# Optimization experiments

Hardware: AMD Instinct MI355X
Metric: run time of the kernel (lower is better)

The kernel has to match this reference:

```python
import jax, jax.numpy as jnp
import numpy as np

D_MODEL = 1024
N_HEADS = 16
D_HEAD = D_MODEL // N_HEADS


def setup_inputs() -> dict:
    key = jax.random.key(0)
    k1, k2, k3, k4, k5 = jax.random.split(key, 5)
    B, S = 2, 2048
    scale_in = 1.0 / np.sqrt(D_MODEL)
    return {
        "x": jax.random.normal(k1, (B, S, D_MODEL), dtype=jnp.float32),
        "qkv_w": jax.random.normal(k2, (3 * D_MODEL, D_MODEL), dtype=jnp.float32) * scale_in,
        "qkv_b": jax.random.normal(k3, (3 * D_MODEL,), dtype=jnp.float32) * 0.02,
        "out_w": jax.random.normal(k4, (D_MODEL, D_MODEL), dtype=jnp.float32) * scale_in,
        "out_b": jax.random.normal(k5, (D_MODEL,), dtype=jnp.float32) * 0.02,
    }


def reference(x, qkv_w, qkv_b, out_w, out_b) -> jnp.ndarray:
    B, S, D = x.shape
    # qkv projection: torch Linear stores weight as (out, in)
    qkv = x @ qkv_w.T + qkv_b                      # [B,S,3D]
    qkv = qkv.reshape(B, S, 3, N_HEADS, D_HEAD)
    qkv = jnp.transpose(qkv, (2, 0, 3, 1, 4))      # [3,B,H,S,d]
    q, k, v = qkv[0], qkv[1], qkv[2]
    scale = 1.0 / np.sqrt(D_HEAD).astype(np.float32)
    scores = jnp.einsum("bhsd,bhtd->bhst", q, k) * scale  # [B,H,S,S]
    attn = jax.nn.softmax(scores, axis=-1)
    out = jnp.einsum("bhst,bhtd->bhsd", attn, v)   # [B,H,S,d]
    out = jnp.transpose(out, (0, 2, 1, 3)).reshape(B, S, D)
    return out @ out_w.T + out_b
```

## Files before the change

### kernel.cpp

```cpp
#include <hip/hip_runtime.h>

typedef __bf16 bf16;
typedef __bf16 bf16x4 __attribute__((ext_vector_type(4)));
typedef __bf16 bf16x8 __attribute__((ext_vector_type(8)));
typedef float  f32x4  __attribute__((ext_vector_type(4)));

__device__ __forceinline__ void gld16(const void* g, void* l) {
  __builtin_amdgcn_global_load_lds(
      (const __attribute__((address_space(1))) void*)g,
      (__attribute__((address_space(3))) void*)l, 16, 0, 0);
}

__global__ void f2bf_all(const float* __restrict__ x, bf16* __restrict__ xo,
                         const float* __restrict__ w1, bf16* __restrict__ w1o,
                         const float* __restrict__ w2, bf16* __restrict__ w2o) {
  int i = blockIdx.x * blockDim.x + threadIdx.x;
  const float* in; bf16* out; int idx;
  if (i < 1048576)      { in = x;  out = xo;  idx = i; }
  else if (i < 1835008) { in = w1; out = w1o; idx = i - 1048576; }
  else                  { in = w2; out = w2o; idx = i - 1835008; }
  float4 v = reinterpret_cast<const float4*>(in)[idx];
  bf16x4 o = { (bf16)v.x, (bf16)v.y, (bf16)v.z, (bf16)v.w };
  reinterpret_cast<bf16x4*>(out)[idx] = o;
}

template<int MODE, int BN>
__global__ __launch_bounds__(256)
void gemm_bt(const bf16* __restrict__ A, const bf16* __restrict__ B,
             const float* __restrict__ bias, void* __restrict__ Cout,
             int K, int N) {
  __shared__ bf16 As[128 * 64];
  __shared__ bf16 Bs[BN * 64];
  const int tid  = threadIdx.x;
  const int wave = tid >> 6, lane = tid & 63;
  const int quad = lane >> 4, l16 = lane & 15;
  const int bm = blockIdx.x * 128, bn = blockIdx.y * BN;
  constexpr int NI  = (BN == 128) ? 4 : 2;
  constexpr int BCH = BN / 32;
  const int wr = (BN == 128) ? (wave >> 1) * 64 : wave * 32;
  const int wc = (BN == 128) ? (wave & 1) * 64 : 0;
  const int arow = lane >> 3;
  const int acol = (lane & 7) * 8;

  f32x4 acc[NI][4] = {};

  const bf16* Ab = A + (size_t)bm * K;
  const bf16* Bb = B + (size_t)bn * K;

  for (int k0 = 0; k0 < K; k0 += 64) {
#pragma unroll
    for (int i = 0; i < 4; ++i) {
      int c = wave * 4 + i;
      gld16(Ab + (size_t)(c * 8 + arow) * K + k0 + acol, As + c * 512);
    }
#pragma unroll
    for (int i = 0; i < BCH; ++i) {
      int c = wave * BCH + i;
      gld16(Bb + (size_t)(c * 8 + arow) * K + k0 + acol, Bs + c * 512);
    }
    __syncthreads();
#pragma unroll
    for (int kk = 0; kk < 64; kk += 32) {
      bf16x8 af[NI], bfr[4];
#pragma unroll
      for (int i = 0; i < NI; ++i)
        af[i]  = *(const bf16x8*)(As + (wr + i * 16 + l16) * 64 + kk + quad * 8);
#pragma unroll
      for (int j = 0; j < 4; ++j)
        bfr[j] = *(const bf16x8*)(Bs + (wc + j * 16 + l16) * 64 + kk + quad * 8);
#pragma unroll
      for (int i = 0; i < NI; ++i)
#pragma unroll
        for (int j = 0; j < 4; ++j)
          acc[i][j] = __builtin_amdgcn_mfma_f32_16x16x32_bf16(af[i], bfr[j], acc[i][j], 0, 0, 0);
    }
    __syncthreads();
  }

  if constexpr (MODE == 0) {
    bf16* Q = (bf16*)Cout;
#pragma unroll
    for (int j = 0; j < 4; ++j) {
      int col = bn + wc + j * 16 + l16;
      float bv  = bias[col];
      int sec = col >> 10, rem = col & 1023;
      int h = rem >> 6, d = rem & 63;
      if (sec < 2) {
        float scl = (sec == 0) ? 0.125f * 1.44269504f : 1.0f;
#pragma unroll
        for (int i = 0; i < NI; ++i) {
#pragma unroll
          for (int r = 0; r < 4; ++r) {
            int row = bm + wr + i * 16 + quad * 4 + r;
            int b = row >> 11, si = row & 2047;
            float v = (acc[i][j][r] + bv) * scl;
            Q[(((size_t)sec * 32 + b * 16 + h) * 2048 + si) * 64 + d] = (bf16)v;
          }
        }
      } else {
#pragma unroll
        for (int i = 0; i < NI; ++i) {
          int row0 = bm + wr + i * 16 + quad * 4;
          int b = row0 >> 11, si = row0 & 2047;
          bf16x4 pk = { (bf16)(acc[i][j][0] + bv), (bf16)(acc[i][j][1] + bv),
                        (bf16)(acc[i][j][2] + bv), (bf16)(acc[i][j][3] + bv) };
          *(bf16x4*)(Q + (size_t)2 * 4194304 +
                     ((size_t)(b * 16 + h) * 64 + d) * 2048 + si) = pk;
        }
      }
    }
  } else {
    float* C = (float*)Cout;
#pragma unroll
    for (int j = 0; j < 4; ++j) {
      int col = bn + wc + j * 16 + l16;
      float bv = bias[col];
#pragma unroll
      for (int i = 0; i < NI; ++i)
#pragma unroll
        for (int r = 0; r < 4; ++r) {
          int row = bm + wr + i * 16 + quad * 4 + r;
          C[(size_t)row * N + col] = acc[i][j][r] + bv;
        }
    }
  }
}

__global__ __launch_bounds__(256, 2)
void attn_kernel(const bf16* __restrict__ QKV, const bf16* __restrict__ Vt,
                 bf16* __restrict__ O) {
  __shared__ bf16 Ks[128 * 72];
  __shared__ bf16 Ps[4][32 * 136];

  const int bh = blockIdx.x;
  const int q0 = blockIdx.y * 128;
  const bf16* Qg = QKV + ((size_t)bh * 2048 + q0) * 64;
  const bf16* Kg = QKV + (size_t)32 * 2048 * 64 + (size_t)bh * 2048 * 64;
  const bf16* Vg = Vt + (size_t)bh * 64 * 2048;

  const int tid  = threadIdx.x;
  const int wave = tid >> 6, lane = tid & 63;
  const int quad = lane >> 4, l16 = lane & 15;
  const int srow = tid >> 3;
  const int scol = (tid & 7) * 8;
  bf16* Pw = &Ps[wave][0];

  bf16x8 aq[2][2];
#pragma unroll
  for (int i = 0; i < 2; ++i)
#pragma unroll
    for (int kh = 0; kh < 2; ++kh)
      aq[i][kh] = *(const bf16x8*)(Qg + (size_t)(wave * 32 + i * 16 + l16) * 64 +
                                   kh * 32 + quad * 8);

  {
    bf16x8 kreg[4];
#pragma unroll
    for (int ch = 0; ch < 4; ++ch)
      kreg[ch] = *(const bf16x8*)(Kg + (size_t)(ch * 32 + srow) * 64 + scol);
#pragma unroll
    for (int ch = 0; ch < 4; ++ch)
      *(bf16x8*)(&Ks[(ch * 32 + srow) * 72 + scol]) = kreg[ch];
  }
  __syncthreads();

  float rs[2] = {0.f, 0.f};
  f32x4 o[2][4] = {};

  for (int kt = 0; kt < 16; ++kt) {
    bf16x8 kreg[4];
    if (kt < 15) {
#pragma unroll
      for (int ch = 0; ch < 4; ++ch)
        kreg[ch] = *(const bf16x8*)(Kg + (size_t)((kt + 1) * 128 + ch * 32 + srow) * 64 + scol);
    }
    bf16x8 bv[4][4];
#pragma unroll
    for (int kk = 0; kk < 4; ++kk)
#pragma unroll
      for (int oj = 0; oj < 4; ++oj)
        bv[kk][oj] = *(const bf16x8*)(Vg + (size_t)(oj * 16 + l16) * 2048 +
                                      kt * 128 + kk * 32 + quad * 8);

    f32x4 s[2][8] = {};
#pragma unroll
    for (int kh = 0; kh < 2; ++kh) {
#pragma unroll
      for (int ni = 0; ni < 8; ++ni) {
        bf16x8 bk = *(const bf16x8*)(&Ks[(ni * 16 + l16) * 72 + kh * 32 + quad * 8]);
        s[0][ni] = __builtin_amdgcn_mfma_f32_16x16x32_bf16(bk, aq[0][kh], s[0][ni], 0, 0, 0);
        s[1][ni] = __builtin_amdgcn_mfma_f32_16x16x32_bf16(bk, aq[1][kh], s[1][ni], 0, 0, 0);
      }
    }

    __syncthreads();

    if (kt < 15) {
#pragma unroll
      for (int ch = 0; ch < 4; ++ch)
        *(bf16x8*)(&Ks[(ch * 32 + srow) * 72 + scol]) = kreg[ch];
    }

#pragma unroll
    for (int i = 0; i < 2; ++i)
#pragma unroll
      for (int ni = 0; ni < 8; ++ni) {
        float p0 = __builtin_amdgcn_exp2f(s[i][ni][0]);
        float p1 = __builtin_amdgcn_exp2f(s[i][ni][1]);
        float p2 = __builtin_amdgcn_exp2f(s[i][ni][2]);
        float p3 = __builtin_amdgcn_exp2f(s[i][ni][3]);
        rs[i] += (p0 + p1) + (p2 + p3);
        bf16x4 pk = { (bf16)p0, (bf16)p1, (bf16)p2, (bf16)p3 };
        *(bf16x4*)(Pw + (i * 16 + l16) * 136 + ni * 16 + quad * 4) = pk;
      }

#pragma unroll
    for (int kk = 0; kk < 4; ++kk) {
#pragma unroll
      for (int i = 0; i < 2; ++i) {
        bf16x8 ap = *(const bf16x8*)(Pw + (i * 16 + l16) * 136 + kk * 32 + quad * 8);
#pragma unroll
        for (int oj = 0; oj < 4; ++oj)
          o[i][oj] = __builtin_amdgcn_mfma_f32_16x16x32_bf16(ap, bv[kk][oj], o[i][oj], 0, 0, 0);
      }
    }

    __syncthreads();
  }

#pragma unroll
  for (int i = 0; i < 2; ++i) {
    rs[i] += __shfl_xor(rs[i], 16);
    rs[i] += __shfl_xor(rs[i], 32);
  }

  const int b = bh >> 4, h = bh & 15;
#pragma unroll
  for (int i = 0; i < 2; ++i)
#pragma unroll
    for (int r = 0; r < 4; ++r) {
      float lsum = __shfl(rs[i], quad * 4 + r);
      float inv = 1.0f / lsum;
      int row = q0 + wave * 32 + i * 16 + quad * 4 + r;
#pragma unroll
      for (int oj = 0; oj < 4; ++oj)
        O[((size_t)(b * 2048 + row)) * 1024 + h * 64 + oj * 16 + l16] =
            (bf16)(o[i][oj][r] * inv);
    }
}

extern "C" void kernel_launch(void* const* d_in, const int* in_sizes, int n_in,
                              void* d_out, int out_size, void* d_ws, size_t ws_size,
                              hipStream_t stream) {
  const float* x      = (const float*)d_in[0];
  const float* qkv_w  = (const float*)d_in[1];
  const float* qkv_b  = (const float*)d_in[2];
  const float* out_w  = (const float*)d_in[3];
  const float* out_b  = (const float*)d_in[4];
  float* out = (float*)d_out;

  char* ws = (char*)d_ws;
  bf16* Xb   = (bf16*)(ws);
  bf16* Wqkv = (bf16*)(ws + 8388608);
  bf16* Wout = (bf16*)(ws + 14680064);
  bf16* QKV  = (bf16*)(ws + 16777216);
  bf16* At   = (bf16*)(ws + 41943040);
  bf16* VtP  = QKV + (size_t)2 * 32 * 2048 * 64;

  f2bf_all<<<8192, 256, 0, stream>>>(x, Xb, qkv_w, Wqkv, out_w, Wout);

  gemm_bt<0, 128><<<dim3(32, 24), 256, 0, stream>>>(Xb, Wqkv, qkv_b, (void*)QKV, 1024, 3072);

  attn_kernel<<<dim3(32, 16), 256, 0, stream>>>(QKV, VtP, At);

  gemm_bt<1, 64><<<dim3(32, 16), 256, 0, stream>>>(At, Wout, out_b, (void*)out, 1024, 1024);
}
```

Before: 225.9 us.

## Split attention over key halves with separate combine kernel

Splits the attention kernel's key dimension into two halves along a new grid z-dimension, doubling the block count from 512 to 1024. Each half writes unnormalized fp32 partial outputs and row sums to workspace, and a new combine kernel sums them, normalizes and writes bf16. It also shrinks the per-wave P buffer in LDS by processing P in two chunks, which should allow higher occupancy. The aim is better CU utilization on the 256-CU part; the cost is extra global traffic for the fp32 partials and one more kernel launch.

```diff
diff --git a/kernel.cpp b/kernel.cpp
--- a/kernel.cpp
+++ b/kernel.cpp
@@ -128,15 +128,19 @@
 
 __global__ __launch_bounds__(256, 2)
 void attn_kernel(const bf16* __restrict__ QKV, const bf16* __restrict__ Vt,
-                 bf16* __restrict__ O) {
+                 float* __restrict__ Opart, float* __restrict__ lpart) {
   __shared__ bf16 Ks[128 * 72];
-  __shared__ bf16 Ps[4][32 * 136];
+  __shared__ bf16 Ps[4][32 * 72];
 
   const int bh = blockIdx.x;
   const int q0 = blockIdx.y * 128;
+  const int half = blockIdx.z;
+  const int kt0 = half * 8;
   const bf16* Qg = QKV + ((size_t)bh * 2048 + q0) * 64;
   const bf16* Kg = QKV + (size_t)32 * 2048 * 64 + (size_t)bh * 2048 * 64;
   const bf16* Vg = Vt + (size_t)bh * 64 * 2048;
+  float* Oh = Opart + (size_t)half * 4194304 + (size_t)bh * 2048 * 64;
+  float* lh = lpart + (size_t)half * 65536 + (size_t)bh * 2048;
 
   const int tid  = threadIdx.x;
   const int wave = tid >> 6, lane = tid & 63;
@@ -157,7 +161,7 @@
     bf16x8 kreg[4];
 #pragma unroll
     for (int ch = 0; ch < 4; ++ch)
-      kreg[ch] = *(const bf16x8*)(Kg + (size_t)(ch * 32 + srow) * 64 + scol);
+      kreg[ch] = *(const bf16x8*)(Kg + (size_t)(kt0 * 128 + ch * 32 + srow) * 64 + scol);
 #pragma unroll
     for (int ch = 0; ch < 4; ++ch)
       *(bf16x8*)(&Ks[(ch * 32 + srow) * 72 + scol]) = kreg[ch];
@@ -167,12 +171,14 @@
   float rs[2] = {0.f, 0.f};
   f32x4 o[2][4] = {};
 
-  for (int kt = 0; kt < 16; ++kt) {
+  for (int kt = 0; kt < 8; ++kt) {
+    const int g = kt0 + kt;
+
     bf16x8 kreg[4];
-    if (kt < 15) {
+    if (kt < 7) {
 #pragma unroll
       for (int ch = 0; ch < 4; ++ch)
-        kreg[ch] = *(const bf16x8*)(Kg + (size_t)((kt + 1) * 128 + ch * 32 + srow) * 64 + scol);
+        kreg[ch] = *(const bf16x8*)(Kg + (size_t)((g + 1) * 128 + ch * 32 + srow) * 64 + scol);
     }
     bf16x8 bv[4][4];
 #pragma unroll
@@ -180,7 +186,7 @@
 #pragma unroll
       for (int oj = 0; oj < 4; ++oj)
         bv[kk][oj] = *(const bf16x8*)(Vg + (size_t)(oj * 16 + l16) * 2048 +
-                                      kt * 128 + kk * 32 + quad * 8);
+                                      g * 128 + kk * 32 + quad * 8);
 
     f32x4 s[2][8] = {};
 #pragma unroll
@@ -195,33 +201,37 @@
 
     __syncthreads();
 
-    if (kt < 15) {
+    if (kt < 7) {
 #pragma unroll
       for (int ch = 0; ch < 4; ++ch)
         *(bf16x8*)(&Ks[(ch * 32 + srow) * 72 + scol]) = kreg[ch];
     }
 
 #pragma unroll
-    for (int i = 0; i < 2; ++i)
-#pragma unroll
-      for (int ni = 0; ni < 8; ++ni) {
-        float p0 = __builtin_amdgcn_exp2f(s[i][ni][0]);
-        float p1 = __builtin_amdgcn_exp2f(s[i][ni][1]);
-        float p2 = __builtin_amdgcn_exp2f(s[i][ni][2]);
-        float p3 = __builtin_amdgcn_exp2f(s[i][ni][3]);
-        rs[i] += (p0 + p1) + (p2 + p3);
-        bf16x4 pk = { (bf16)p0, (bf16)p1, (bf16)p2, (bf16)p3 };
-        *(bf16x4*)(Pw + (i * 16 + l16) * 136 + ni * 16 + quad * 4) = pk;
-      }
-
-#pragma unroll
-    for (int kk = 0; kk < 4; ++kk) {
-#pragma unroll
-      for (int i = 0; i < 2; ++i) {
-        bf16x8 ap = *(const bf16x8*)(Pw + (i * 16 + l16) * 136 + kk * 32 + quad * 8);
-#pragma unroll
-        for (int oj = 0; oj < 4; ++oj)
-          o[i][oj] = __builtin_amdgcn_mfma_f32_16x16x32_bf16(ap, bv[kk][oj], o[i][oj], 0, 0, 0);
+    for (int c = 0; c < 2; ++c) {
+#pragma unroll
+      for (int i = 0; i < 2; ++i)
+#pragma unroll
+        for (int nc = 0; nc < 4; ++nc) {
+          int ni = c * 4 + nc;
+          float p0 = __builtin_amdgcn_exp2f(s[i][ni][0]);
+          float p1 = __builtin_amdgcn_exp2f(s[i][ni][1]);
+          float p2 = __builtin_amdgcn_exp2f(s[i][ni][2]);
+          float p3 = __builtin_amdgcn_exp2f(s[i][ni][3]);
+          rs[i] += (p0 + p1) + (p2 + p3);
+          bf16x4 pk = { (bf16)p0, (bf16)p1, (bf16)p2, (bf16)p3 };
+          *(bf16x4*)(Pw + (i * 16 + l16) * 72 + nc * 16 + quad * 4) = pk;
+        }
+#pragma unroll
+      for (int kc = 0; kc < 2; ++kc) {
+        int kk = c * 2 + kc;
+#pragma unroll
+        for (int i = 0; i < 2; ++i) {
+          bf16x8 ap = *(const bf16x8*)(Pw + (i * 16 + l16) * 72 + kc * 32 + quad * 8);
+#pragma unroll
+          for (int oj = 0; oj < 4; ++oj)
+            o[i][oj] = __builtin_amdgcn_mfma_f32_16x16x32_bf16(ap, bv[kk][oj], o[i][oj], 0, 0, 0);
+        }
       }
     }
 
@@ -234,19 +244,33 @@
     rs[i] += __shfl_xor(rs[i], 32);
   }
 
-  const int b = bh >> 4, h = bh & 15;
-#pragma unroll
-  for (int i = 0; i < 2; ++i)
+#pragma unroll
+  for (int i = 0; i < 2; ++i) {
+    if (quad == 0)
+      lh[q0 + wave * 32 + i * 16 + l16] = rs[i];
 #pragma unroll
     for (int r = 0; r < 4; ++r) {
-      float lsum = __shfl(rs[i], quad * 4 + r);
-      float inv = 1.0f / lsum;
       int row = q0 + wave * 32 + i * 16 + quad * 4 + r;
 #pragma unroll
       for (int oj = 0; oj < 4; ++oj)
-        O[((size_t)(b * 2048 + row)) * 1024 + h * 64 + oj * 16 + l16] =
-            (bf16)(o[i][oj][r] * inv);
-    }
+        Oh[(size_t)row * 64 + oj * 16 + l16] = o[i][oj][r];
+    }
+  }
+}
+
+__global__ void attn_combine(const float* __restrict__ O0, const float* __restrict__ O1,
+                             const float* __restrict__ l0, const float* __restrict__ l1,
+                             bf16* __restrict__ At) {
+  int i = blockIdx.x * blockDim.x + threadIdx.x;
+  int rid = i >> 4, d4 = i & 15;
+  float inv = 1.0f / (l0[rid] + l1[rid]);
+  f32x4 a = reinterpret_cast<const f32x4*>(O0)[i];
+  f32x4 b = reinterpret_cast<const f32x4*>(O1)[i];
+  int bh = rid >> 11, s = rid & 2047;
+  int bb = bh >> 4, h = bh & 15;
+  bf16x4 ov = { (bf16)((a[0] + b[0]) * inv), (bf16)((a[1] + b[1]) * inv),
+                (bf16)((a[2] + b[2]) * inv), (bf16)((a[3] + b[3]) * inv) };
+  *reinterpret_cast<bf16x4*>(At + ((size_t)(bb * 2048 + s)) * 1024 + h * 64 + d4 * 4) = ov;
 }
 
 extern "C" void kernel_launch(void* const* d_in, const int* in_sizes, int n_in,
@@ -260,18 +284,23 @@
   float* out = (float*)d_out;
 
   char* ws = (char*)d_ws;
-  bf16* Xb   = (bf16*)(ws);
-  bf16* Wqkv = (bf16*)(ws + 8388608);
-  bf16* Wout = (bf16*)(ws + 14680064);
-  bf16* QKV  = (bf16*)(ws + 16777216);
-  bf16* At   = (bf16*)(ws + 41943040);
-  bf16* VtP  = QKV + (size_t)2 * 32 * 2048 * 64;
+  bf16* Xb    = (bf16*)(ws);
+  bf16* Wqkv  = (bf16*)(ws + 8388608);
+  bf16* Wout  = (bf16*)(ws + 14680064);
+  bf16* QKV   = (bf16*)(ws + 16777216);
+  bf16* At    = (bf16*)(ws + 41943040);
+  float* Opart = (float*)(ws + 50331648);
+  float* lpart = (float*)(ws + 83886080);
+  bf16* VtP   = QKV + (size_t)2 * 32 * 2048 * 64;
 
   f2bf_all<<<8192, 256, 0, stream>>>(x, Xb, qkv_w, Wqkv, out_w, Wout);
 
   gemm_bt<0, 128><<<dim3(32, 24), 256, 0, stream>>>(Xb, Wqkv, qkv_b, (void*)QKV, 1024, 3072);
 
-  attn_kernel<<<dim3(32, 16), 256, 0, stream>>>(QKV, VtP, At);
+  attn_kernel<<<dim3(32, 16, 2), 256, 0, stream>>>(QKV, VtP, Opart, lpart);
+
+  attn_combine<<<4096, 256, 0, stream>>>(Opart, Opart + 4194304,
+                                         lpart, lpart + 65536, At);
 
   gemm_bt<1, 64><<<dim3(32, 16), 256, 0, stream>>>(At, Wout, out_b, (void*)out, 1024, 1024);
 }
```

Result: slower. 233.4 us (+3.3%).

## Software-pipeline attention in half-tiles with swizzled async K loads

Applied to the files above, without the earlier changes.

Splits each 128-key tile into two 64-key halves and interleaves the second half's QK^T MFMAs with the first half's exp/P store, so matrix and vector work overlap. K tiles are now loaded straight into LDS with global_load_lds, using an XOR swizzle in place of row padding to avoid bank conflicts, and the P buffer shrinks to half width. This frees the registers that held K during the copy and shrinks LDS, at the cost of more complex scheduling and extra barriers per tile.

```diff
diff --git a/kernel.cpp b/kernel.cpp
--- a/kernel.cpp
+++ b/kernel.cpp
@@ -129,8 +129,8 @@
 __global__ __launch_bounds__(256, 2)
 void attn_kernel(const bf16* __restrict__ QKV, const bf16* __restrict__ Vt,
                  bf16* __restrict__ O) {
-  __shared__ bf16 Ks[128 * 72];
-  __shared__ bf16 Ps[4][32 * 136];
+  __shared__ bf16 Ks[128 * 64];
+  __shared__ bf16 Ps[4][32 * 72];
 
   const int bh = blockIdx.x;
   const int q0 = blockIdx.y * 128;
@@ -142,7 +142,8 @@
   const int wave = tid >> 6, lane = tid & 63;
   const int quad = lane >> 4, l16 = lane & 15;
   const int srow = tid >> 3;
-  const int scol = (tid & 7) * 8;
+  const int swcol = ((tid & 7) * 8) ^ ((srow & 7) << 3);
+  const int xrd = (l16 & 7) << 3;
   bf16* Pw = &Ps[wave][0];
 
   bf16x8 aq[2][2];
@@ -153,79 +154,97 @@
       aq[i][kh] = *(const bf16x8*)(Qg + (size_t)(wave * 32 + i * 16 + l16) * 64 +
                                    kh * 32 + quad * 8);
 
-  {
-    bf16x8 kreg[4];
-#pragma unroll
-    for (int ch = 0; ch < 4; ++ch)
-      kreg[ch] = *(const bf16x8*)(Kg + (size_t)(ch * 32 + srow) * 64 + scol);
-#pragma unroll
-    for (int ch = 0; ch < 4; ++ch)
-      *(bf16x8*)(&Ks[(ch * 32 + srow) * 72 + scol]) = kreg[ch];
-  }
-  __syncthreads();
-
   float rs[2] = {0.f, 0.f};
   f32x4 o[2][4] = {};
 
-  for (int kt = 0; kt < 16; ++kt) {
-    bf16x8 kreg[4];
-    if (kt < 15) {
+  auto QK = [&](f32x4 s[2][4], int g, int c) {
+#pragma unroll
+    for (int kh = 0; kh < 2; ++kh)
+#pragma unroll
+      for (int nc = 0; nc < 4; ++nc) {
+        int row = (c * 4 + nc) * 16 + l16;
+        bf16x8 bk = *(const bf16x8*)(&Ks[row * 64 + ((kh * 32 + quad * 8) ^ xrd)]);
+        s[0][nc] = __builtin_amdgcn_mfma_f32_16x16x32_bf16(bk, aq[0][kh], s[0][nc], 0, 0, 0);
+        s[1][nc] = __builtin_amdgcn_mfma_f32_16x16x32_bf16(bk, aq[1][kh], s[1][nc], 0, 0, 0);
+      }
+  };
+  auto LDV = [&](bf16x8 bv[2][4], int g, int c) {
+#pragma unroll
+    for (int kc = 0; kc < 2; ++kc)
+#pragma unroll
+      for (int oj = 0; oj < 4; ++oj)
+        bv[kc][oj] = *(const bf16x8*)(Vg + (size_t)(oj * 16 + l16) * 2048 +
+                                      g * 128 + (c * 2 + kc) * 32 + quad * 8);
+  };
+  auto SMcol = [&](f32x4 s[2][4], int nc) {
+#pragma unroll
+    for (int i = 0; i < 2; ++i) {
+      float p0 = __builtin_amdgcn_exp2f(s[i][nc][0]);
+      float p1 = __builtin_amdgcn_exp2f(s[i][nc][1]);
+      float p2 = __builtin_amdgcn_exp2f(s[i][nc][2]);
+      float p3 = __builtin_amdgcn_exp2f(s[i][nc][3]);
+      rs[i] += (p0 + p1) + (p2 + p3);
+      bf16x4 pk = { (bf16)p0, (bf16)p1, (bf16)p2, (bf16)p3 };
+      *(bf16x4*)(Pw + (i * 16 + l16) * 72 + nc * 16 + quad * 4) = pk;
+    }
+  };
+  auto PV = [&](bf16x8 bv[2][4]) {
+#pragma unroll
+    for (int kc = 0; kc < 2; ++kc)
+#pragma unroll
+      for (int i = 0; i < 2; ++i) {
+        bf16x8 ap = *(const bf16x8*)(Pw + (i * 16 + l16) * 72 + kc * 32 + quad * 8);
+#pragma unroll
+        for (int oj = 0; oj < 4; ++oj)
+          o[i][oj] = __builtin_amdgcn_mfma_f32_16x16x32_bf16(ap, bv[kc][oj], o[i][oj], 0, 0, 0);
+      }
+  };
+
+#pragma unroll
+  for (int ch = 0; ch < 4; ++ch)
+    gld16(Kg + (size_t)(0 * 128 + ch * 32 + srow) * 64 + swcol,
+          Ks + ch * 2048 + wave * 512);
+  __syncthreads();
+
+  bf16x8 bv0[2][4], bv1[2][4];
+  f32x4 s_cur[2][4] = {}, s_nxt[2][4];
+  LDV(bv0, 0, 0);
+  QK(s_cur, 0, 0);
+
+  for (int t = 0; t < 16; ++t) {
+    LDV(bv1, t, 1);
+#pragma unroll
+    for (int nc = 0; nc < 4; ++nc) s_nxt[0][nc] = f32x4{}, s_nxt[1][nc] = f32x4{};
+#pragma unroll
+    for (int nc = 0; nc < 4; ++nc) {
+#pragma unroll
+      for (int kh = 0; kh < 2; ++kh) {
+        int row = (4 + nc) * 16 + l16;
+        bf16x8 bk = *(const bf16x8*)(&Ks[row * 64 + ((kh * 32 + quad * 8) ^ xrd)]);
+        s_nxt[0][nc] = __builtin_amdgcn_mfma_f32_16x16x32_bf16(bk, aq[0][kh], s_nxt[0][nc], 0, 0, 0);
+        s_nxt[1][nc] = __builtin_amdgcn_mfma_f32_16x16x32_bf16(bk, aq[1][kh], s_nxt[1][nc], 0, 0, 0);
+      }
+      SMcol(s_cur, nc);
+    }
+    PV(bv0);
+
+    __syncthreads();
+    if (t < 15) {
 #pragma unroll
       for (int ch = 0; ch < 4; ++ch)
-        kreg[ch] = *(const bf16x8*)(Kg + (size_t)((kt + 1) * 128 + ch * 32 + srow) * 64 + scol);
-    }
-    bf16x8 bv[4][4];
-#pragma unroll
-    for (int kk = 0; kk < 4; ++kk)
-#pragma unroll
-      for (int oj = 0; oj < 4; ++oj)
-        bv[kk][oj] = *(const bf16x8*)(Vg + (size_t)(oj * 16 + l16) * 2048 +
-                                      kt * 128 + kk * 32 + quad * 8);
-
-    f32x4 s[2][8] = {};
-#pragma unroll
-    for (int kh = 0; kh < 2; ++kh) {
-#pragma unroll
-      for (int ni = 0; ni < 8; ++ni) {
-        bf16x8 bk = *(const bf16x8*)(&Ks[(ni * 16 + l16) * 72 + kh * 32 + quad * 8]);
-        s[0][ni] = __builtin_amdgcn_mfma_f32_16x16x32_bf16(bk, aq[0][kh], s[0][ni], 0, 0, 0);
-        s[1][ni] = __builtin_amdgcn_mfma_f32_16x16x32_bf16(bk, aq[1][kh], s[1][ni], 0, 0, 0);
-      }
-    }
-
-    __syncthreads();
-
-    if (kt < 15) {
-#pragma unroll
-      for (int ch = 0; ch < 4; ++ch)
-        *(bf16x8*)(&Ks[(ch * 32 + srow) * 72 + scol]) = kreg[ch];
-    }
-
-#pragma unroll
-    for (int i = 0; i < 2; ++i)
-#pragma unroll
-      for (int ni = 0; ni < 8; ++ni) {
-        float p0 = __builtin_amdgcn_exp2f(s[i][ni][0]);
-        float p1 = __builtin_amdgcn_exp2f(s[i][ni][1]);
-        float p2 = __builtin_amdgcn_exp2f(s[i][ni][2]);
-        float p3 = __builtin_amdgcn_exp2f(s[i][ni][3]);
-        rs[i] += (p0 + p1) + (p2 + p3);
-        bf16x4 pk = { (bf16)p0, (bf16)p1, (bf16)p2, (bf16)p3 };
-        *(bf16x4*)(Pw + (i * 16 + l16) * 136 + ni * 16 + quad * 4) = pk;
-      }
-
-#pragma unroll
-    for (int kk = 0; kk < 4; ++kk) {
-#pragma unroll
-      for (int i = 0; i < 2; ++i) {
-        bf16x8 ap = *(const bf16x8*)(Pw + (i * 16 + l16) * 136 + kk * 32 + quad * 8);
-#pragma unroll
-        for (int oj = 0; oj < 4; ++oj)
-          o[i][oj] = __builtin_amdgcn_mfma_f32_16x16x32_bf16(ap, bv[kk][oj], o[i][oj], 0, 0, 0);
-      }
-    }
-
-    __syncthreads();
+        gld16(Kg + (size_t)((t + 1) * 128 + ch * 32 + srow) * 64 + swcol,
+              Ks + ch * 2048 + wave * 512);
+    }
+#pragma unroll
+    for (int nc = 0; nc < 4; ++nc) SMcol(s_nxt, nc);
+    PV(bv1);
+    if (t < 15) {
+      __syncthreads();
+      LDV(bv0, t + 1, 0);
+#pragma unroll
+      for (int nc = 0; nc < 4; ++nc) s_cur[0][nc] = f32x4{}, s_cur[1][nc] = f32x4{};
+      QK(s_cur, t + 1, 0);
+    }
   }
 
 #pragma unroll
```

Result: no change. 228.1 us (+1.0%).
